# Kernel tuning notes

Measured on AMD Instinct MI355X. Metric: run time of the kernel, lower is better.

## Reference

```python
import jax, jax.numpy as jnp
import numpy as np

B = 8192          # batch rows
C_IN = 4096       # total input channels
G = 8             # number of clusters
CG = C_IN // G    # channels per cluster (arrangement.shape[0])
J = 512           # j_rank per cluster (output width per cluster)


def setup_inputs() -> dict:
    key = jax.random.key(0)
    kx, kp, kw, kb = jax.random.split(key, 4)
    x = jax.random.normal(kx, (B, C_IN), dtype=jnp.float32)
    # arrangements: a random permutation of all input channels split into G groups,
    # mimicking channel-clustering assignments (each channel used exactly once)
    perm = jax.random.permutation(kp, C_IN)
    arrangements = perm.reshape(G, CG).astype(jnp.int64)
    # per-group nn.Linear weights: torch layout (out_features, in_features)
    weights = jax.random.normal(kw, (G, J, CG), dtype=jnp.float32) * (1.0 / np.sqrt(CG))
    bias = jax.random.normal(kb, (G, J), dtype=jnp.float32) * 0.02
    return {"x": x, "arrangements": arrangements, "weights": weights, "bias": bias}


def reference(x, arrangements, weights, bias):
    # Gather each cluster's channels: x[:, arrangements] -> [B, G, CG]
    xg = jnp.take(x, arrangements, axis=1)
    # Per-group linear (torch Linear: y = x @ W.T + b), batched over groups,
    # then concat along feature dim -> [B, G*J]
    out = jnp.einsum('bgc,gjc->bgj', xg, weights) + bias[None, :, :]
    return out.reshape(x.shape[0], -1)
```

## Files before the change

### kernel.cpp

```cpp
#include <hip/hip_runtime.h>
#include <hip/hip_bf16.h>

#define B_ROWS 8192
#define C_IN   4096
#define G_GRP  8
#define CG     512
#define J_RANK 512

#define BM 128
#define BN 128
#define BK 32
#define NKT (CG / BK)

#define RPB    8
#define PERM_BLOCKS (B_ROWS / RPB)
#define CONV_BLOCKS 128

typedef __attribute__((ext_vector_type(8))) short bf16x8;
typedef __attribute__((ext_vector_type(4))) float f32x4;
typedef __attribute__((ext_vector_type(8))) unsigned short u16x8;

struct ushort4v { unsigned short x, y, z, w; };

__device__ __forceinline__ unsigned short f2bf(float f) {
    unsigned int u = __float_as_uint(f);
    unsigned int r = (u + 0x7FFFu + ((u >> 16) & 1u)) >> 16;
    return (unsigned short)r;
}

__global__ __launch_bounds__(256) void permute_x_kernel(
    const float* __restrict__ x, const int* __restrict__ arr,
    unsigned short* __restrict__ xp,
    const float* __restrict__ w, unsigned short* __restrict__ wb) {
    const int tid = threadIdx.x;

    if (blockIdx.x >= PERM_BLOCKS) {
        const int cb = blockIdx.x - PERM_BLOCKS;
#pragma unroll
        for (int t = 0; t < 16; ++t) {
            int i = cb * 4096 + t * 256 + tid;
            float4 v = ((const float4*)w)[i];
            ushort4v o;
            o.x = f2bf(v.x); o.y = f2bf(v.y); o.z = f2bf(v.z); o.w = f2bf(v.w);
            ((ushort4v*)wb)[i] = o;
        }
        return;
    }

    __shared__ float buf[2][C_IN];
    const int row0 = blockIdx.x * RPB;

    const bool is64 = (arr[1] == 0 && arr[3] == 0 && arr[5] == 0 && arr[7] == 0);

    int sidx[16];
#pragma unroll
    for (int pass = 0; pass < 2; ++pass)
#pragma unroll
        for (int k = 0; k < 8; ++k) {
            int p = pass * 2048 + tid * 8 + k;
            sidx[pass * 8 + k] = is64 ? arr[2 * p] : arr[p];
        }

    float4 ra[4], rb[4];

#define PLOAD(dst_, r_)                                                      \
    do {                                                                     \
        const float4* s_ = (const float4*)(x + (size_t)(row0 + (r_)) * C_IN);\
        _Pragma("unroll")                                                    \
        for (int i_ = 0; i_ < 4; ++i_) dst_[i_] = s_[i_ * 256 + tid];        \
    } while (0)

#define PROW(regs_, r_)                                                      \
    do {                                                                     \
        float4* d_ = (float4*)&buf[(r_) & 1][0];                             \
        _Pragma("unroll")                                                    \
        for (int i_ = 0; i_ < 4; ++i_) d_[i_ * 256 + tid] = regs_[i_];       \
        asm volatile("s_waitcnt lgkmcnt(0)" ::: "memory");                   \
        __builtin_amdgcn_s_barrier();          \
        const float* bi_ = &buf[(r_) & 1][0];                                \
        unsigned short* orow_ = xp + (size_t)(row0 + (r_)) * C_IN;           \
        _Pragma("unroll")                                                    \
        for (int pass_ = 0; pass_ < 2; ++pass_) {                            \
            u16x8 o_;                                                        \
            _Pragma("unroll")                                                \
            for (int k_ = 0; k_ < 8; ++k_)                                   \
                o_[k_] = f2bf(bi_[sidx[pass_ * 8 + k_]]);                    \
            *(u16x8*)(orow_ + pass_ * 2048 + tid * 8) = o_;                  \
        }                                                                    \
    } while (0)

    PLOAD(ra, 0);
#pragma unroll
    for (int r = 0; r < RPB; ++r) {
        if (r & 1) {
            if (r + 1 < RPB) PLOAD(ra, r + 1);
            PROW(rb, r);
        } else {
            if (r + 1 < RPB) PLOAD(rb, r + 1);
            PROW(ra, r);
        }
    }
#undef PLOAD
#undef PROW
}

__global__ __launch_bounds__(256, 4) void gemm_kernel(
    const unsigned short* __restrict__ Xp,
    const unsigned short* __restrict__ Wb,
    const float* __restrict__ bias,
    float* __restrict__ out) {
    __shared__ unsigned short ldsA[3][BM * BK];
    __shared__ unsigned short ldsB[2][BN * BK];

    const int tid = threadIdx.x;
    const int g   = blockIdx.x & 7;
    const int idx = blockIdx.x >> 3;
    const int mt  = idx >> 2;
    const int nt  = idx & 3;

    const int l   = tid & 63;
    const int wv  = tid >> 6;
    const int wr  = wv >> 1;
    const int wc  = wv & 1;
    const int lr  = l & 15;
    const int lkq = l >> 4;

    const unsigned short* Ab = Xp + (size_t)(mt * BM) * C_IN + g * CG;
    const unsigned short* Bb = Wb + (size_t)g * J_RANK * CG + (size_t)(nt * BN) * CG;

    f32x4 acc[4][4];
#pragma unroll
    for (int m = 0; m < 4; ++m)
#pragma unroll
        for (int n = 0; n < 4; ++n) acc[m][n] = (f32x4){0.f, 0.f, 0.f, 0.f};

    const int coff = (lkq ^ ((lr >> 2) & 3)) * 8;

#define STAGE_A(kt_)                                                          \
    do { const int p_ = (kt_) % 3;                                            \
        _Pragma("unroll")                                                     \
        for (int i_ = 0; i_ < 2; ++i_) {                                      \
            int c_ = i_ * 256 + tid;                                          \
            int rl_ = c_ >> 2, gc_ = (c_ & 3) ^ ((rl_ >> 2) & 3);             \
            __builtin_amdgcn_global_load_lds(                                 \
                (const __attribute__((address_space(1))) unsigned int*)       \
                    (Ab + (size_t)rl_ * C_IN + (kt_) * BK + gc_ * 8),         \
                (__attribute__((address_space(3))) unsigned int*)             \
                    (&ldsA[p_][0] + c_ * 8),                                  \
                16, 0, 0);                                                    \
        }                                                                     \
    } while (0)

#define STAGE_B(kt_)                                                          \
    do { const int p_ = (kt_) & 1;                                            \
        _Pragma("unroll")                                                     \
        for (int i_ = 0; i_ < 2; ++i_) {                                      \
            int c_ = i_ * 256 + tid;                                          \
            int rl_ = c_ >> 2, gc_ = (c_ & 3) ^ ((rl_ >> 2) & 3);             \
            __builtin_amdgcn_global_load_lds(                                 \
                (const __attribute__((address_space(1))) unsigned int*)       \
                    (Bb + (size_t)rl_ * CG + (kt_) * BK + gc_ * 8),           \
                (__attribute__((address_space(3))) unsigned int*)             \
                    (&ldsB[p_][0] + c_ * 8),                                  \
                16, 0, 0);                                                    \
        }                                                                     \
    } while (0)

#define LDA(m_) (*(const bf16x8*)&ldsA[bufA][(wr * 64 + (m_) * 16 + lr) * BK + coff])
#define LDB(n_) (*(const bf16x8*)&ldsB[bufB][(wc * 64 + (n_) * 16 + lr) * BK + coff])

#define PHASE_TAIL()                                                          \
    __builtin_amdgcn_s_barrier();                                             \
    asm volatile("s_waitcnt lgkmcnt(0)" ::: "memory");                        \
    __builtin_amdgcn_sched_barrier(0);                                        \
    __builtin_amdgcn_s_setprio(1)

#define PHASE_END()                                                           \
    __builtin_amdgcn_s_setprio(0);                                            \
    __builtin_amdgcn_s_barrier()

    STAGE_A(0); STAGE_B(0);
    STAGE_A(1);
    asm volatile("s_waitcnt vmcnt(2)" ::: "memory");
    __builtin_amdgcn_s_barrier();

    bf16x8 bfr[4], af[2];

    for (int kt = 0; kt < NKT; ++kt) {
        const int bufA = kt % 3;
        const int bufB = kt & 1;

#pragma unroll
        for (int n = 0; n < 4; ++n) bfr[n] = LDB(n);
        af[0] = LDA(0); af[1] = LDA(1);
        if (kt + 1 < NKT) STAGE_B(kt + 1);
        if (kt + 2 < NKT) STAGE_A(kt + 2);
        PHASE_TAIL();
#pragma unroll
        for (int mm = 0; mm < 2; ++mm)
#pragma unroll
            for (int n = 0; n < 4; ++n)
                acc[mm][n] = __builtin_amdgcn_mfma_f32_16x16x32_bf16(
                    af[mm], bfr[n], acc[mm][n], 0, 0, 0);
        PHASE_END();

        af[0] = LDA(2); af[1] = LDA(3);
        if (kt <= NKT - 3)      asm volatile("s_waitcnt vmcnt(2)" ::: "memory");
        else                    asm volatile("s_waitcnt vmcnt(0)" ::: "memory");
        PHASE_TAIL();
#pragma unroll
        for (int mm = 0; mm < 2; ++mm)
#pragma unroll
            for (int n = 0; n < 4; ++n)
                acc[2 + mm][n] = __builtin_amdgcn_mfma_f32_16x16x32_bf16(
                    af[mm], bfr[n], acc[2 + mm][n], 0, 0, 0);
        PHASE_END();
    }
#undef STAGE_A
#undef STAGE_B
#undef LDA
#undef LDB
#undef PHASE_TAIL
#undef PHASE_END

    const int r0 = mt * BM + wr * 64 + (lkq << 2);
    const int cbase = nt * BN + wc * 64 + lr;
#pragma unroll
    for (int n = 0; n < 4; ++n) {
        int col = cbase + n * 16;
        float bv = bias[g * J_RANK + col];
#pragma unroll
        for (int m = 0; m < 4; ++m) {
            int row = r0 + m * 16;
            float* op = out + (size_t)row * C_IN + g * J_RANK + col;
#pragma unroll
            for (int r = 0; r < 4; ++r)
                __builtin_nontemporal_store(acc[m][n][r] + bv,
                                            op + (size_t)r * C_IN);
        }
    }
}

extern "C" void kernel_launch(void* const* d_in, const int* in_sizes, int n_in,
                              void* d_out, int out_size, void* d_ws, size_t ws_size,
                              hipStream_t stream) {
    const float* x    = (const float*)d_in[0];
    const int*   arr  = (const int*)d_in[1];
    const float* w    = (const float*)d_in[2];
    const float* bias = (const float*)d_in[3];
    float* out = (float*)d_out;

    unsigned short* xp = (unsigned short*)d_ws;
    unsigned short* wb = xp + (size_t)B_ROWS * C_IN;

    hipLaunchKernelGGL(permute_x_kernel, dim3(PERM_BLOCKS + CONV_BLOCKS),
                       dim3(256), 0, stream, x, arr, xp, w, wb);
    hipLaunchKernelGGL(gemm_kernel,
                       dim3(G_GRP * (B_ROWS / BM) * (J_RANK / BN)), dim3(256),
                       0, stream, xp, wb, bias, out);
}
```

Before: 91.66 us.

## Collapse two-phase ping-pong GEMM loop into single phase with one barrier

Replaces the two half-iteration phases, each with its own barrier pair, lgkmcnt wait and sched_barrier, with a single phase per k-tile. All four A fragments and four B fragments are loaded up front, all 16 MFMAs are issued under raised priority, and one vmcnt wait plus barrier closes the iteration. The aim is to cut barrier and wait overhead from four barriers to one per k-step. The trade-off is more live VGPRs for A fragments and the loss of the explicit wave-interleaved schedule that overlapped LDS reads with MFMAs.

```diff
diff --git a/kernel.cpp b/kernel.cpp
--- a/kernel.cpp
+++ b/kernel.cpp
@@ -169,22 +169,13 @@
 #define LDA(m_) (*(const bf16x8*)&ldsA[bufA][(wr * 64 + (m_) * 16 + lr) * BK + coff])
 #define LDB(n_) (*(const bf16x8*)&ldsB[bufB][(wc * 64 + (n_) * 16 + lr) * BK + coff])
 
-#define PHASE_TAIL()                                                          \
-    __builtin_amdgcn_s_barrier();                                             \
-    asm volatile("s_waitcnt lgkmcnt(0)" ::: "memory");                        \
-    __builtin_amdgcn_sched_barrier(0);                                        \
-    __builtin_amdgcn_s_setprio(1)
-
-#define PHASE_END()                                                           \
-    __builtin_amdgcn_s_setprio(0);                                            \
-    __builtin_amdgcn_s_barrier()
-
     STAGE_A(0); STAGE_B(0);
     STAGE_A(1);
     asm volatile("s_waitcnt vmcnt(2)" ::: "memory");
     __builtin_amdgcn_s_barrier();
-
-    bf16x8 bfr[4], af[2];
+    __builtin_amdgcn_sched_barrier(0);
+
+    bf16x8 bfr[4], af[4];
 
     for (int kt = 0; kt < NKT; ++kt) {
         const int bufA = kt % 3;
@@ -192,36 +183,32 @@
 
 #pragma unroll
         for (int n = 0; n < 4; ++n) bfr[n] = LDB(n);
-        af[0] = LDA(0); af[1] = LDA(1);
+#pragma unroll
+        for (int m = 0; m < 4; ++m) af[m] = LDA(m);
+
         if (kt + 1 < NKT) STAGE_B(kt + 1);
         if (kt + 2 < NKT) STAGE_A(kt + 2);
-        PHASE_TAIL();
-#pragma unroll
-        for (int mm = 0; mm < 2; ++mm)
+
+        __builtin_amdgcn_s_setprio(1);
+#pragma unroll
+        for (int m = 0; m < 4; ++m)
 #pragma unroll
             for (int n = 0; n < 4; ++n)
-                acc[mm][n] = __builtin_amdgcn_mfma_f32_16x16x32_bf16(
-                    af[mm], bfr[n], acc[mm][n], 0, 0, 0);
-        PHASE_END();
-
-        af[0] = LDA(2); af[1] = LDA(3);
-        if (kt <= NKT - 3)      asm volatile("s_waitcnt vmcnt(2)" ::: "memory");
-        else                    asm volatile("s_waitcnt vmcnt(0)" ::: "memory");
-        PHASE_TAIL();
-#pragma unroll
-        for (int mm = 0; mm < 2; ++mm)
-#pragma unroll
-            for (int n = 0; n < 4; ++n)
-                acc[2 + mm][n] = __builtin_amdgcn_mfma_f32_16x16x32_bf16(
-                    af[mm], bfr[n], acc[2 + mm][n], 0, 0, 0);
-        PHASE_END();
+                acc[m][n] = __builtin_amdgcn_mfma_f32_16x16x32_bf16(
+                    af[m], bfr[n], acc[m][n], 0, 0, 0);
+        __builtin_amdgcn_s_setprio(0);
+
+        if (kt + 1 < NKT) {
+            if (kt <= NKT - 3) asm volatile("s_waitcnt vmcnt(2)" ::: "memory");
+            else               asm volatile("s_waitcnt vmcnt(0)" ::: "memory");
+            __builtin_amdgcn_s_barrier();
+            __builtin_amdgcn_sched_barrier(0);
+        }
     }
 #undef STAGE_A
 #undef STAGE_B
 #undef LDA
 #undef LDB
-#undef PHASE_TAIL
-#undef PHASE_END
 
     const int r0 = mt * BM + wr * 64 + (lkq << 2);
     const int cbase = nt * BN + wc * 64 + lr;
```

After: 92.11 us. About the same (+0.5%).
